# Kernel optimization log

Measured on AMD Instinct MI355X. Metric: run time of the kernel, lower is better.

The kernel has to match this reference:

```python
import jax, jax.numpy as jnp
import numpy as np

D_MODEL = 1024
N_HEADS = 16
D_K = D_MODEL // N_HEADS  # 64
SCALE = 1.0 / np.sqrt(D_K).astype(np.float32)


def setup_inputs() -> dict:
    key = jax.random.key(0)
    kx, kq, kk, kv, ko = jax.random.split(key, 5)
    B, S = 2, 2048
    s = 0.02  # keep pre-softmax logits in a sane range
    return {
        "x": jax.random.normal(kx, (B, S, D_MODEL), dtype=jnp.float32),
        "Wq": jax.random.normal(kq, (D_MODEL, D_MODEL), dtype=jnp.float32) * s,
        "Wk": jax.random.normal(kk, (D_MODEL, D_MODEL), dtype=jnp.float32) * s,
        "Wv": jax.random.normal(kv, (D_MODEL, D_MODEL), dtype=jnp.float32) * s,
        "Wo": jax.random.normal(ko, (D_MODEL, D_MODEL), dtype=jnp.float32) * s,
    }


def reference(x, Wq, Wk, Wv, Wo):
    # x: [B, S, D]; nn.Linear(bias=False) computes x @ W.T
    B, S, D = x.shape
    H, dk = N_HEADS, D_K

    def proj(W):
        # [B, S, D] -> [B, H, S, dk]
        return (x @ W.T).reshape(B, S, H, dk).transpose(0, 2, 1, 3)

    q = proj(Wq)
    k = proj(Wk)
    v = proj(Wv)

    # Flash tiling with online softmax is exact full attention (no mask):
    scores = jnp.einsum("bhqd,bhkd->bhqk", q, k) * SCALE  # [B,H,S,S]
    p = jax.nn.softmax(scores, axis=-1)
    o = jnp.einsum("bhqk,bhkd->bhqd", p, v)               # [B,H,S,dk]

    o = o.transpose(0, 2, 1, 3).reshape(B, S, D)
    return o @ Wo.T
```

## Files before the change

### kernel.cpp

```cpp
#include <hip/hip_runtime.h>
#include <cstdint>
#include <type_traits>

typedef __attribute__((ext_vector_type(8))) __bf16 bf16x8;
typedef __attribute__((ext_vector_type(4))) float f32x4;
using u16 = unsigned short;
using u32 = unsigned int;

#define D_MODEL 1024
#define N_HEADS 16
#define D_K     64
#define SEQ     2048
#define BATCH   2
#define NTOKENS (BATCH * SEQ)
#define SCALE   0.125f
#define LOG2E   1.44269504088896340736f
#define C2      (SCALE * LOG2E)

__device__ __forceinline__ u16 f32_to_bf16(float f) {
    union { float f; u32 u; } v; v.f = f;
    u32 r = (v.u + 0x7fffu + ((v.u >> 16) & 1u)) >> 16;
    return (u16)r;
}

__device__ __forceinline__ u32 pack_bf16_pair(float a, float b) {
    u32 ua = __builtin_bit_cast(u32, a) + 0x8000u;
    u32 ub = __builtin_bit_cast(u32, b) + 0x8000u;
    return __builtin_amdgcn_perm(ub, ua, 0x07060302);
}

typedef const __attribute__((address_space(1))) u32* gas_ptr;
typedef __attribute__((address_space(3))) u32* las_ptr;
__device__ __forceinline__ void gl2lds16(const u16* g, u16* l) {
    __builtin_amdgcn_global_load_lds((gas_ptr)g, (las_ptr)l, 16, 0, 0);
}

__global__ __launch_bounds__(256) void cvt_all(const float* __restrict__ x,
                                               const float* __restrict__ Wq, const float* __restrict__ Wk,
                                               const float* __restrict__ Wv, const float* __restrict__ Wo,
                                               u16* __restrict__ xb,
                                               u16* __restrict__ wq, u16* __restrict__ wk,
                                               u16* __restrict__ wv, u16* __restrict__ wo) {
    const int NX = NTOKENS * D_MODEL;
    size_t i = (size_t)(blockIdx.x * 256 + threadIdx.x) * 4;
    const float* src; u16* dst; size_t off;
    if (i < (size_t)NX) { src = x; dst = xb; off = i; }
    else {
        size_t j = i - NX;
        int w = (int)(j >> 20);
        off = j & ((1u << 20) - 1);
        src = (w == 0) ? Wq : (w == 1) ? Wk : (w == 2) ? Wv : Wo;
        dst = (w == 0) ? wq : (w == 1) ? wk : (w == 2) ? wv : wo;
    }
    float4 f = *(const float4*)(src + off);
    u32 lo = (u32)f32_to_bf16(f.x) | ((u32)f32_to_bf16(f.y) << 16);
    u32 hi = (u32)f32_to_bf16(f.z) | ((u32)f32_to_bf16(f.w) << 16);
    uint2 o; o.x = lo; o.y = hi;
    *(uint2*)(dst + off) = o;
}

__global__ __launch_bounds__(256) void gemm_qkv(const u16* __restrict__ xb,
                                                const u16* __restrict__ wq,
                                                const u16* __restrict__ wk,
                                                const u16* __restrict__ wv,
                                                u16* __restrict__ Qb, u16* __restrict__ Kb,
                                                u16* __restrict__ Vt) {
    __shared__ __align__(16) u16 As[2][128 * 32];
    __shared__ __align__(16) u16 Bs[2][128 * 32];

    const int tid  = threadIdx.x;
    const int wave = tid >> 6, lane = tid & 63;
    const int quad = lane >> 4, l4 = lane & 15;
    const int wm = wave >> 1, wn = wave & 1;
    const int f = blockIdx.x;

    const u16 *Abase, *Bbase;
    if (f < 512) {
        const int m0 = (f & 31) * 128, t = f >> 5;
        Abase = xb + (size_t)m0 * D_MODEL;
        Bbase = ((t < 8) ? wq : wk) + (size_t)(t & 7) * 128 * D_MODEL;
    } else {
        const int g = f - 512;
        Abase = wv + (size_t)(g & 7) * 128 * D_MODEL;
        Bbase = xb + (size_t)(g >> 3) * 128 * D_MODEL;
    }

    f32x4 acc[4][4] = {};

    const int r0 = wave * 16 + (lane >> 2);
    const int ch = (lane & 3) * 8;
    const u16* Ag0 = Abase + (size_t)r0 * D_MODEL + ch;
    const u16* Bg0 = Bbase + (size_t)r0 * D_MODEL + ch;
    u16* AsW0 = As[0] + wave * 512;
    u16* AsW1 = As[1] + wave * 512;
    u16* BsW0 = Bs[0] + wave * 512;
    u16* BsW1 = Bs[1] + wave * 512;

    for (int kt = 0; kt < 16; ++kt) {
        const int ko = kt * 64;
        __syncthreads();
        gl2lds16(Ag0 + ko, AsW0);
        gl2lds16(Ag0 + (size_t)64 * D_MODEL + ko, AsW0 + 2048);
        gl2lds16(Bg0 + ko, BsW0);
        gl2lds16(Bg0 + (size_t)64 * D_MODEL + ko, BsW0 + 2048);
        gl2lds16(Ag0 + ko + 32, AsW1);
        gl2lds16(Ag0 + (size_t)64 * D_MODEL + ko + 32, AsW1 + 2048);
        gl2lds16(Bg0 + ko + 32, BsW1);
        gl2lds16(Bg0 + (size_t)64 * D_MODEL + ko + 32, BsW1 + 2048);
        __syncthreads();

#pragma unroll
        for (int s = 0; s < 2; ++s) {
            bf16x8 af[4], bfr[4];
#pragma unroll
            for (int mt = 0; mt < 4; mt++)
                af[mt] = *(const bf16x8*)&As[s][(wm * 64 + mt * 16 + l4) * 32 + quad * 8];
#pragma unroll
            for (int nt = 0; nt < 4; nt++)
                bfr[nt] = *(const bf16x8*)&Bs[s][(wn * 64 + nt * 16 + l4) * 32 + quad * 8];
#pragma unroll
            for (int mt = 0; mt < 4; mt++)
#pragma unroll
                for (int nt = 0; nt < 4; nt++)
                    acc[mt][nt] = __builtin_amdgcn_mfma_f32_16x16x32_bf16(af[mt], bfr[nt], acc[mt][nt], 0, 0, 0);
        }
    }

#pragma unroll
    for (int mt = 0; mt < 4; mt++)
#pragma unroll
        for (int nt = 0; nt < 4; nt++)
#pragma unroll
            for (int r = 0; r < 4; r++) {
                int mrow = wm * 64 + mt * 16 + quad * 4 + r;
                int ncol = wn * 64 + nt * 16 + l4;
                float v = acc[mt][nt][r];
                if (f < 512) {
                    const int m0 = (f & 31) * 128, t = f >> 5;
                    if (t < 8)
                        Qb[(size_t)(m0 + mrow) * D_MODEL + (t & 7) * 128 + ncol] = f32_to_bf16(v * C2);
                    else
                        Kb[(size_t)(m0 + mrow) * D_MODEL + (t & 7) * 128 + ncol] = f32_to_bf16(v);
                } else {
                    const int g = f - 512;
                    Vt[(size_t)((g & 7) * 128 + mrow) * NTOKENS + (g >> 3) * 128 + ncol] = f32_to_bf16(v);
                }
            }
}

__global__ __launch_bounds__(256) void gemm_out(const u16* __restrict__ A,
                                                const u16* __restrict__ Bw,
                                                float* __restrict__ C) {
    __shared__ __align__(16) u16 As[64 * 32];
    __shared__ __align__(16) u16 Bs[128 * 32];

    const int tid  = threadIdx.x;
    const int wave = tid >> 6, lane = tid & 63;
    const int quad = lane >> 4, l4 = lane & 15;
    const int m0 = blockIdx.y * 64, n0 = blockIdx.x * 128;

    f32x4 acc[4][2] = {};

    const int r0 = wave * 16 + (lane >> 2);
    const int ch = (lane & 3) * 8;
    const u16* Ag0 = A  + (size_t)(m0 + r0) * D_MODEL + ch;
    const u16* Bg0 = Bw + (size_t)(n0 + r0) * D_MODEL + ch;
    u16* AsW = As + wave * 512;
    u16* BsW = Bs + wave * 512;

    for (int kt = 0; kt < 32; ++kt) {
        const int ko = kt * 32;
        __syncthreads();
        gl2lds16(Ag0 + ko, AsW);
        gl2lds16(Bg0 + ko, BsW);
        gl2lds16(Bg0 + (size_t)64 * D_MODEL + ko, BsW + 2048);
        __syncthreads();

        bf16x8 af[4], bfr[2];
#pragma unroll
        for (int mt = 0; mt < 4; mt++)
            af[mt] = *(const bf16x8*)&As[(mt * 16 + l4) * 32 + quad * 8];
#pragma unroll
        for (int nt = 0; nt < 2; nt++)
            bfr[nt] = *(const bf16x8*)&Bs[(wave * 32 + nt * 16 + l4) * 32 + quad * 8];
#pragma unroll
        for (int mt = 0; mt < 4; mt++)
#pragma unroll
            for (int nt = 0; nt < 2; nt++)
                acc[mt][nt] = __builtin_amdgcn_mfma_f32_16x16x32_bf16(af[mt], bfr[nt], acc[mt][nt], 0, 0, 0);
    }

#pragma unroll
    for (int mt = 0; mt < 4; mt++)
#pragma unroll
        for (int nt = 0; nt < 2; nt++)
#pragma unroll
            for (int r = 0; r < 4; r++) {
                int m = m0 + mt * 16 + quad * 4 + r;
                int n = n0 + wave * 32 + nt * 16 + l4;
                C[(size_t)m * D_MODEL + n] = acc[mt][nt][r];
            }
}

__global__ __launch_bounds__(512, 4) void attn(const u16* __restrict__ Q,
                                               const u16* __restrict__ K,
                                               const u16* __restrict__ Vt,
                                               u16* __restrict__ O) {
    __shared__ __align__(16) u16 smem[2 * 64 * 72 + 2 * 80 * 72];
    u16* KsB = smem;
    u16* VsB = smem + 2 * 64 * 72;
    const int KBUF = 64 * 72, VBUF = 80 * 72;

    const int tid  = threadIdx.x;
    const int wave = tid >> 6, lane = tid & 63;
    const int quad = lane >> 4, l4 = lane & 15;
    const int qg = wave & 3, kv = wave >> 2;
    const int bid = blockIdx.x;
    const int h  = (bid & 7) | (((bid >> 3) & 1) << 3);
    const int b  = (bid >> 4) & 1;
    const int q0 = (bid >> 5) * 128;
    const size_t headoff = (size_t)b * SEQ * D_MODEL + (size_t)h * D_K;

    for (int i = tid; i < 2 * 16 * 72; i += 512) {
        int buf = i / (16 * 72), rem = i % (16 * 72);
        VsB[buf * VBUF + (64 + rem / 72) * 72 + (rem % 72)] = (rem / 72 == 0) ? (u16)0x3F80 : (u16)0;
    }

    const int sarr = tid >> 8;
    const int st   = tid & 255;
    const int srow = st >> 2, sc = st & 3;
    const u16* gsrc = (sarr == 0)
        ? K  + headoff + (size_t)srow * D_MODEL + sc * 16
        : Vt + (size_t)(h * 64 + srow) * NTOKENS + (size_t)b * SEQ + sc * 16;
    const size_t gstep = (sarr == 0) ? (size_t)64 * D_MODEL : 64;
    u16* kw0 = KsB + srow * 72 + sc * 16;
    u16* vw0 = VsB + srow * 72 + (sc >> 1) * 32 + (sc & 1) * 4;

    bf16x8 qa[2][2];
#pragma unroll
    for (int qs = 0; qs < 2; qs++) {
        const u16* qp = Q + headoff + (size_t)(q0 + qg * 32 + qs * 16 + l4) * D_MODEL + quad * 8;
        qa[qs][0] = *(const bf16x8*)qp;
        qa[qs][1] = *(const bf16x8*)(qp + 32);
    }

    int4 pr0 = *(const int4*)gsrc;
    int4 pr1 = *(const int4*)(gsrc + 8);

    f32x4 acc_o[2][4] = {};
    f32x4 acc_l[2] = {};

    for (int it = 0; it < 32; ++it) {
        if (sarr == 0) {
            u16* d = kw0 + (it & 1) * KBUF;
            *(int4*)d       = pr0;
            *(int4*)(d + 8) = pr1;
        } else {
            u16* d = vw0 + (it & 1) * VBUF;
            const uint2* h0 = (const uint2*)&pr0;
            const uint2* h1 = (const uint2*)&pr1;
            *(uint2*)(d)      = h0[0];
            *(uint2*)(d + 8)  = h0[1];
            *(uint2*)(d + 16) = h1[0];
            *(uint2*)(d + 24) = h1[1];
        }
        __syncthreads();

        const u16* gn = gsrc + (size_t)((it + 1) & 31) * gstep;
        pr0 = *(const int4*)gn;
        pr1 = *(const int4*)(gn + 8);

        const u16* ksr = KsB + (it & 1) * KBUF;
        const u16* vsr = VsB + (it & 1) * VBUF;

        f32x4 sacc[2][2] = {};
#pragma unroll
        for (int n2 = 0; n2 < 2; n2++) {
            const int krow = kv * 32 + n2 * 16 + l4;
            bf16x8 kb0 = *(const bf16x8*)&ksr[krow * 72 + quad * 8];
            bf16x8 kb1 = *(const bf16x8*)&ksr[krow * 72 + 32 + quad * 8];
#pragma unroll
            for (int qs = 0; qs < 2; qs++) {
                sacc[qs][n2] = __builtin_amdgcn_mfma_f32_16x16x32_bf16(kb0, qa[qs][0], sacc[qs][n2], 0, 0, 0);
                sacc[qs][n2] = __builtin_amdgcn_mfma_f32_16x16x32_bf16(kb1, qa[qs][1], sacc[qs][n2], 0, 0, 0);
            }
        }

        union { u32 u[4]; bf16x8 v; } pp[2];
#pragma unroll
        for (int qs = 0; qs < 2; qs++)
#pragma unroll
            for (int n2 = 0; n2 < 2; n2++) {
                float p0 = __builtin_amdgcn_exp2f(sacc[qs][n2][0]);
                float p1 = __builtin_amdgcn_exp2f(sacc[qs][n2][1]);
                float p2 = __builtin_amdgcn_exp2f(sacc[qs][n2][2]);
                float p3 = __builtin_amdgcn_exp2f(sacc[qs][n2][3]);
                pp[qs].u[n2 * 2]     = pack_bf16_pair(p0, p1);
                pp[qs].u[n2 * 2 + 1] = pack_bf16_pair(p2, p3);
            }

#pragma unroll
        for (int dvt = 0; dvt < 4; dvt++) {
            bf16x8 vfr = *(const bf16x8*)&vsr[(dvt * 16 + l4) * 72 + kv * 32 + quad * 8];
#pragma unroll
            for (int qs = 0; qs < 2; qs++)
                acc_o[qs][dvt] = __builtin_amdgcn_mfma_f32_16x16x32_bf16(pp[qs].v, vfr, acc_o[qs][dvt], 0, 0, 0);
        }
        {
            bf16x8 ofr = *(const bf16x8*)&vsr[(64 + l4) * 72 + kv * 32 + quad * 8];
#pragma unroll
            for (int qs = 0; qs < 2; qs++)
                acc_l[qs] = __builtin_amdgcn_mfma_f32_16x16x32_bf16(pp[qs].v, ofr, acc_l[qs], 0, 0, 0);
        }
    }

    float* Of = (float*)smem;
    float* Lf = (float*)(smem + 16384);
    __syncthreads();
    if (kv == 1) {
#pragma unroll
        for (int qs = 0; qs < 2; qs++) {
#pragma unroll
            for (int dvt = 0; dvt < 4; dvt++)
#pragma unroll
                for (int r = 0; r < 4; r++)
                    Of[(qg * 32 + qs * 16 + quad * 4 + r) * 64 + dvt * 16 + l4] = acc_o[qs][dvt][r];
            if (l4 == 0)
#pragma unroll
                for (int r = 0; r < 4; r++)
                    Lf[qg * 32 + qs * 16 + quad * 4 + r] = acc_l[qs][r];
        }
    }
    __syncthreads();
    if (kv == 0) {
#pragma unroll
        for (int qs = 0; qs < 2; qs++)
#pragma unroll
            for (int r = 0; r < 4; r++) {
                float lown = __shfl(acc_l[qs][r], quad * 16, 64);
                float ltot = lown + Lf[qg * 32 + qs * 16 + quad * 4 + r];
                float linv = 1.f / ltot;
                int qrow = q0 + qg * 32 + qs * 16 + quad * 4 + r;
#pragma unroll
                for (int dvt = 0; dvt < 4; dvt++) {
                    float v = acc_o[qs][dvt][r] +
                              Of[(qg * 32 + qs * 16 + quad * 4 + r) * 64 + dvt * 16 + l4];
                    O[headoff + (size_t)qrow * D_MODEL + dvt * 16 + l4] = f32_to_bf16(v * linv);
                }
            }
    }
}

extern "C" void kernel_launch(void* const* d_in, const int* in_sizes, int n_in,
                              void* d_out, int out_size, void* d_ws, size_t ws_size,
                              hipStream_t stream) {
    const float* x  = (const float*)d_in[0];
    const float* Wq = (const float*)d_in[1];
    const float* Wk = (const float*)d_in[2];
    const float* Wv = (const float*)d_in[3];
    const float* Wo = (const float*)d_in[4];

    const int NW = D_MODEL * D_MODEL;

    char* ws = (char*)d_ws;
    u16* xb = (u16*)ws;
    u16* wq = (u16*)(ws + (8u << 20));
    u16* wk = wq + NW;
    u16* wv = wk + NW;
    u16* wo = wv + NW;
    u16* Qb  = (u16*)(ws + (16u << 20));
    u16* Kb  = (u16*)(ws + (24u << 20));
    u16* Vtb = (u16*)(ws + (32u << 20));

    cvt_all<<<8192, 256, 0, stream>>>(x, Wq, Wk, Wv, Wo, xb, wq, wk, wv, wo);

    gemm_qkv<<<768, 256, 0, stream>>>(xb, wq, wk, wv, Qb, Kb, Vtb);

    attn<<<512, 512, 0, stream>>>(Qb, Kb, Vtb, xb);

    gemm_out<<<dim3(8, 64), 256, 0, stream>>>(xb, wo, (float*)d_out);
}
```

Baseline: 188.8 us.

## Retile attention and output GEMM, use hardware bf16 pack and MFMA priority

The attention kernel moves from 512-thread blocks (4 query groups × 2 KV halves) to 256-thread blocks in which each wave handles all 64 queries of a block against its own quarter of a 128-key tile. The row-sum now uses a register ones vector instead of extra LDS rows, and the partial sums of the four waves are reduced in two stages. The output GEMM grows to 128x128 tiles with a 64-wide K step staged in two LDS halves, and the attention kernel uses v_cvt_pk_bf16_f32 plus s_setprio around its MFMA blocks. The aim is more operand reuse per LDS read and fewer loop iterations and barriers, at the cost of higher register pressure and lower occupancy.

```diff
diff --git a/kernel.cpp b/kernel.cpp
--- a/kernel.cpp
+++ b/kernel.cpp
@@ -1,6 +1,5 @@
 #include <hip/hip_runtime.h>
 #include <cstdint>
-#include <type_traits>
 
 typedef __attribute__((ext_vector_type(8))) __bf16 bf16x8;
 typedef __attribute__((ext_vector_type(4))) float f32x4;
@@ -23,10 +22,10 @@
     return (u16)r;
 }
 
-__device__ __forceinline__ u32 pack_bf16_pair(float a, float b) {
-    u32 ua = __builtin_bit_cast(u32, a) + 0x8000u;
-    u32 ub = __builtin_bit_cast(u32, b) + 0x8000u;
-    return __builtin_amdgcn_perm(ub, ua, 0x07060302);
+__device__ __forceinline__ u32 cvt_pk_bf16(float a, float b) {
+    u32 r;
+    asm("v_cvt_pk_bf16_f32 %0, %1, %2" : "=v"(r) : "v"(a), "v"(b));
+    return r;
 }
 
 typedef const __attribute__((address_space(1))) u32* gas_ptr;
@@ -151,200 +150,264 @@
 __global__ __launch_bounds__(256) void gemm_out(const u16* __restrict__ A,
                                                 const u16* __restrict__ Bw,
                                                 float* __restrict__ C) {
-    __shared__ __align__(16) u16 As[64 * 32];
-    __shared__ __align__(16) u16 Bs[128 * 32];
+    __shared__ __align__(16) u16 As[2][128 * 32];
+    __shared__ __align__(16) u16 Bs[2][128 * 32];
 
     const int tid  = threadIdx.x;
     const int wave = tid >> 6, lane = tid & 63;
     const int quad = lane >> 4, l4 = lane & 15;
-    const int m0 = blockIdx.y * 64, n0 = blockIdx.x * 128;
-
-    f32x4 acc[4][2] = {};
+    const int wm = wave >> 1, wn = wave & 1;
+    const int m0 = (blockIdx.x & 31) * 128, n0 = (blockIdx.x >> 5) * 128;
+
+    f32x4 acc[4][4] = {};
 
     const int r0 = wave * 16 + (lane >> 2);
     const int ch = (lane & 3) * 8;
     const u16* Ag0 = A  + (size_t)(m0 + r0) * D_MODEL + ch;
     const u16* Bg0 = Bw + (size_t)(n0 + r0) * D_MODEL + ch;
-    u16* AsW = As + wave * 512;
-    u16* BsW = Bs + wave * 512;
-
-    for (int kt = 0; kt < 32; ++kt) {
-        const int ko = kt * 32;
+    u16* AsW0 = As[0] + wave * 512;
+    u16* AsW1 = As[1] + wave * 512;
+    u16* BsW0 = Bs[0] + wave * 512;
+    u16* BsW1 = Bs[1] + wave * 512;
+
+    for (int kt = 0; kt < 16; ++kt) {
+        const int ko = kt * 64;
         __syncthreads();
-        gl2lds16(Ag0 + ko, AsW);
-        gl2lds16(Bg0 + ko, BsW);
-        gl2lds16(Bg0 + (size_t)64 * D_MODEL + ko, BsW + 2048);
+        gl2lds16(Ag0 + ko, AsW0);
+        gl2lds16(Ag0 + (size_t)64 * D_MODEL + ko, AsW0 + 2048);
+        gl2lds16(Bg0 + ko, BsW0);
+        gl2lds16(Bg0 + (size_t)64 * D_MODEL + ko, BsW0 + 2048);
+        gl2lds16(Ag0 + ko + 32, AsW1);
+        gl2lds16(Ag0 + (size_t)64 * D_MODEL + ko + 32, AsW1 + 2048);
+        gl2lds16(Bg0 + ko + 32, BsW1);
+        gl2lds16(Bg0 + (size_t)64 * D_MODEL + ko + 32, BsW1 + 2048);
         __syncthreads();
 
-        bf16x8 af[4], bfr[2];
-#pragma unroll
-        for (int mt = 0; mt < 4; mt++)
-            af[mt] = *(const bf16x8*)&As[(mt * 16 + l4) * 32 + quad * 8];
-#pragma unroll
-        for (int nt = 0; nt < 2; nt++)
-            bfr[nt] = *(const bf16x8*)&Bs[(wave * 32 + nt * 16 + l4) * 32 + quad * 8];
-#pragma unroll
-        for (int mt = 0; mt < 4; mt++)
-#pragma unroll
-            for (int nt = 0; nt < 2; nt++)
-                acc[mt][nt] = __builtin_amdgcn_mfma_f32_16x16x32_bf16(af[mt], bfr[nt], acc[mt][nt], 0, 0, 0);
+#pragma unroll
+        for (int s = 0; s < 2; ++s) {
+            bf16x8 af[4], bfr[4];
+#pragma unroll
+            for (int mt = 0; mt < 4; mt++)
+                af[mt] = *(const bf16x8*)&As[s][(wm * 64 + mt * 16 + l4) * 32 + quad * 8];
+#pragma unroll
+            for (int nt = 0; nt < 4; nt++)
+                bfr[nt] = *(const bf16x8*)&Bs[s][(wn * 64 + nt * 16 + l4) * 32 + quad * 8];
+#pragma unroll
+            for (int mt = 0; mt < 4; mt++)
+#pragma unroll
+                for (int nt = 0; nt < 4; nt++)
+                    acc[mt][nt] = __builtin_amdgcn_mfma_f32_16x16x32_bf16(af[mt], bfr[nt], acc[mt][nt], 0, 0, 0);
+        }
     }
 
 #pragma unroll
     for (int mt = 0; mt < 4; mt++)
 #pragma unroll
-        for (int nt = 0; nt < 2; nt++)
+        for (int nt = 0; nt < 4; nt++)
 #pragma unroll
             for (int r = 0; r < 4; r++) {
-                int m = m0 + mt * 16 + quad * 4 + r;
-                int n = n0 + wave * 32 + nt * 16 + l4;
-                C[(size_t)m * D_MODEL + n] = acc[mt][nt][r];
+                int mrow = wm * 64 + mt * 16 + quad * 4 + r;
+                int ncol = wn * 64 + nt * 16 + l4;
+                C[(size_t)(m0 + mrow) * D_MODEL + n0 + ncol] = acc[mt][nt][r];
             }
 }
 
-__global__ __launch_bounds__(512, 4) void attn(const u16* __restrict__ Q,
+__global__ __launch_bounds__(256, 2) void attn(const u16* __restrict__ Q,
                                                const u16* __restrict__ K,
                                                const u16* __restrict__ Vt,
                                                u16* __restrict__ O) {
-    __shared__ __align__(16) u16 smem[2 * 64 * 72 + 2 * 80 * 72];
+    __shared__ __align__(16) u16 smem[2 * 128 * 72 + 2 * 64 * 136];
     u16* KsB = smem;
-    u16* VsB = smem + 2 * 64 * 72;
-    const int KBUF = 64 * 72, VBUF = 80 * 72;
+    u16* VsB = smem + 2 * 128 * 72;
+    const int KBUF = 128 * 72, VBUF = 64 * 136;
 
     const int tid  = threadIdx.x;
-    const int wave = tid >> 6, lane = tid & 63;
+    const int kv   = tid >> 6, lane = tid & 63;
     const int quad = lane >> 4, l4 = lane & 15;
-    const int qg = wave & 3, kv = wave >> 2;
-    const int bid = blockIdx.x;
-    const int h  = (bid & 7) | (((bid >> 3) & 1) << 3);
-    const int b  = (bid >> 4) & 1;
-    const int q0 = (bid >> 5) * 128;
+    const int bid  = blockIdx.x;
+    const int bh   = bid >> 5;
+    const int b    = bh >> 4, h = bh & 15;
+    const int q0   = (bid & 31) * 64;
     const size_t headoff = (size_t)b * SEQ * D_MODEL + (size_t)h * D_K;
 
-    for (int i = tid; i < 2 * 16 * 72; i += 512) {
-        int buf = i / (16 * 72), rem = i % (16 * 72);
-        VsB[buf * VBUF + (64 + rem / 72) * 72 + (rem % 72)] = (rem / 72 == 0) ? (u16)0x3F80 : (u16)0;
-    }
-
-    const int sarr = tid >> 8;
-    const int st   = tid & 255;
-    const int srow = st >> 2, sc = st & 3;
-    const u16* gsrc = (sarr == 0)
-        ? K  + headoff + (size_t)srow * D_MODEL + sc * 16
-        : Vt + (size_t)(h * 64 + srow) * NTOKENS + (size_t)b * SEQ + sc * 16;
-    const size_t gstep = (sarr == 0) ? (size_t)64 * D_MODEL : 64;
+    const int srow = tid >> 2, sc = tid & 3;
+    const u16* gK = K  + headoff + (size_t)srow * D_MODEL + sc * 16;
+    const u16* gV = Vt + (size_t)(h * 64 + srow) * NTOKENS + (size_t)b * SEQ + sc * 16;
     u16* kw0 = KsB + srow * 72 + sc * 16;
-    u16* vw0 = VsB + srow * 72 + (sc >> 1) * 32 + (sc & 1) * 4;
-
-    bf16x8 qa[2][2];
-#pragma unroll
-    for (int qs = 0; qs < 2; qs++) {
-        const u16* qp = Q + headoff + (size_t)(q0 + qg * 32 + qs * 16 + l4) * D_MODEL + quad * 8;
+    u16* vw0 = VsB + srow * 136 + (sc >> 1) * 32 + (sc & 1) * 4;
+
+    bf16x8 qa[4][2];
+#pragma unroll
+    for (int qs = 0; qs < 4; qs++) {
+        const u16* qp = Q + headoff + (size_t)(q0 + qs * 16 + l4) * D_MODEL + quad * 8;
         qa[qs][0] = *(const bf16x8*)qp;
         qa[qs][1] = *(const bf16x8*)(qp + 32);
     }
 
-    int4 pr0 = *(const int4*)gsrc;
-    int4 pr1 = *(const int4*)(gsrc + 8);
-
-    f32x4 acc_o[2][4] = {};
-    f32x4 acc_l[2] = {};
-
-    for (int it = 0; it < 32; ++it) {
-        if (sarr == 0) {
-            u16* d = kw0 + (it & 1) * KBUF;
-            *(int4*)d       = pr0;
-            *(int4*)(d + 8) = pr1;
-        } else {
-            u16* d = vw0 + (it & 1) * VBUF;
-            const uint2* h0 = (const uint2*)&pr0;
-            const uint2* h1 = (const uint2*)&pr1;
-            *(uint2*)(d)      = h0[0];
-            *(uint2*)(d + 8)  = h0[1];
-            *(uint2*)(d + 16) = h1[0];
-            *(uint2*)(d + 24) = h1[1];
+    union { u32 u[4]; bf16x8 v; } onesu;
+#pragma unroll
+    for (int i = 0; i < 4; i++) onesu.u[i] = 0x3F803F80u;
+
+    int4 pk[4], pv[4];
+    pk[0] = *(const int4*)gK;
+    pk[1] = *(const int4*)(gK + 8);
+    pk[2] = *(const int4*)(gK + (size_t)64 * D_MODEL);
+    pk[3] = *(const int4*)(gK + (size_t)64 * D_MODEL + 8);
+    pv[0] = *(const int4*)gV;
+    pv[1] = *(const int4*)(gV + 8);
+    pv[2] = *(const int4*)(gV + 64);
+    pv[3] = *(const int4*)(gV + 72);
+
+    f32x4 acc_o[4][4] = {};
+    f32x4 acc_l[4] = {};
+
+    for (int it = 0; it < 16; ++it) {
+        u16* kd = kw0 + (it & 1) * KBUF;
+        *(int4*)kd = pk[0];
+        *(int4*)(kd + 8) = pk[1];
+        *(int4*)(kd + 64 * 72) = pk[2];
+        *(int4*)(kd + 64 * 72 + 8) = pk[3];
+        u16* vd = vw0 + (it & 1) * VBUF;
+        {
+            const uint2* a0 = (const uint2*)&pv[0];
+            const uint2* a1 = (const uint2*)&pv[1];
+            *(uint2*)(vd)      = a0[0];
+            *(uint2*)(vd + 8)  = a0[1];
+            *(uint2*)(vd + 16) = a1[0];
+            *(uint2*)(vd + 24) = a1[1];
+            const uint2* b0 = (const uint2*)&pv[2];
+            const uint2* b1 = (const uint2*)&pv[3];
+            u16* vd2 = vd + 64;
+            *(uint2*)(vd2)      = b0[0];
+            *(uint2*)(vd2 + 8)  = b0[1];
+            *(uint2*)(vd2 + 16) = b1[0];
+            *(uint2*)(vd2 + 24) = b1[1];
         }
         __syncthreads();
 
-        const u16* gn = gsrc + (size_t)((it + 1) & 31) * gstep;
-        pr0 = *(const int4*)gn;
-        pr1 = *(const int4*)(gn + 8);
+        const int nx = (it + 1) & 15;
+        const u16* gkn = gK + (size_t)nx * 128 * D_MODEL;
+        const u16* gvn = gV + (size_t)nx * 128;
+        pk[0] = *(const int4*)gkn;
+        pk[1] = *(const int4*)(gkn + 8);
+        pk[2] = *(const int4*)(gkn + (size_t)64 * D_MODEL);
+        pk[3] = *(const int4*)(gkn + (size_t)64 * D_MODEL + 8);
+        pv[0] = *(const int4*)gvn;
+        pv[1] = *(const int4*)(gvn + 8);
+        pv[2] = *(const int4*)(gvn + 64);
+        pv[3] = *(const int4*)(gvn + 72);
 
         const u16* ksr = KsB + (it & 1) * KBUF;
         const u16* vsr = VsB + (it & 1) * VBUF;
 
-        f32x4 sacc[2][2] = {};
+        bf16x8 kb[2][2];
 #pragma unroll
         for (int n2 = 0; n2 < 2; n2++) {
             const int krow = kv * 32 + n2 * 16 + l4;
-            bf16x8 kb0 = *(const bf16x8*)&ksr[krow * 72 + quad * 8];
-            bf16x8 kb1 = *(const bf16x8*)&ksr[krow * 72 + 32 + quad * 8];
-#pragma unroll
-            for (int qs = 0; qs < 2; qs++) {
-                sacc[qs][n2] = __builtin_amdgcn_mfma_f32_16x16x32_bf16(kb0, qa[qs][0], sacc[qs][n2], 0, 0, 0);
-                sacc[qs][n2] = __builtin_amdgcn_mfma_f32_16x16x32_bf16(kb1, qa[qs][1], sacc[qs][n2], 0, 0, 0);
+            kb[n2][0] = *(const bf16x8*)&ksr[krow * 72 + quad * 8];
+            kb[n2][1] = *(const bf16x8*)&ksr[krow * 72 + 32 + quad * 8];
+        }
+        f32x4 sacc[4][2] = {};
+        __builtin_amdgcn_s_setprio(1);
+#pragma unroll
+        for (int qs = 0; qs < 4; qs++)
+#pragma unroll
+            for (int n2 = 0; n2 < 2; n2++) {
+                sacc[qs][n2] = __builtin_amdgcn_mfma_f32_16x16x32_bf16(kb[n2][0], qa[qs][0], sacc[qs][n2], 0, 0, 0);
+                sacc[qs][n2] = __builtin_amdgcn_mfma_f32_16x16x32_bf16(kb[n2][1], qa[qs][1], sacc[qs][n2], 0, 0, 0);
             }
-        }
-
-        union { u32 u[4]; bf16x8 v; } pp[2];
-#pragma unroll
-        for (int qs = 0; qs < 2; qs++)
+        __builtin_amdgcn_s_setprio(0);
+
+        union { u32 u[4]; bf16x8 v; } pp[4];
+#pragma unroll
+        for (int qs = 0; qs < 4; qs++)
 #pragma unroll
             for (int n2 = 0; n2 < 2; n2++) {
                 float p0 = __builtin_amdgcn_exp2f(sacc[qs][n2][0]);
                 float p1 = __builtin_amdgcn_exp2f(sacc[qs][n2][1]);
                 float p2 = __builtin_amdgcn_exp2f(sacc[qs][n2][2]);
                 float p3 = __builtin_amdgcn_exp2f(sacc[qs][n2][3]);
-                pp[qs].u[n2 * 2]     = pack_bf16_pair(p0, p1);
-                pp[qs].u[n2 * 2 + 1] = pack_bf16_pair(p2, p3);
+                pp[qs].u[n2 * 2]     = cvt_pk_bf16(p0, p1);
+                pp[qs].u[n2 * 2 + 1] = cvt_pk_bf16(p2, p3);
             }
 
+        __builtin_amdgcn_s_setprio(1);
 #pragma unroll
         for (int dvt = 0; dvt < 4; dvt++) {
-            bf16x8 vfr = *(const bf16x8*)&vsr[(dvt * 16 + l4) * 72 + kv * 32 + quad * 8];
-#pragma unroll
-            for (int qs = 0; qs < 2; qs++)
+            bf16x8 vfr = *(const bf16x8*)&vsr[(dvt * 16 + l4) * 136 + kv * 32 + quad * 8];
+#pragma unroll
+            for (int qs = 0; qs < 4; qs++)
                 acc_o[qs][dvt] = __builtin_amdgcn_mfma_f32_16x16x32_bf16(pp[qs].v, vfr, acc_o[qs][dvt], 0, 0, 0);
         }
-        {
-            bf16x8 ofr = *(const bf16x8*)&vsr[(64 + l4) * 72 + kv * 32 + quad * 8];
-#pragma unroll
-            for (int qs = 0; qs < 2; qs++)
-                acc_l[qs] = __builtin_amdgcn_mfma_f32_16x16x32_bf16(pp[qs].v, ofr, acc_l[qs], 0, 0, 0);
-        }
-    }
-
-    float* Of = (float*)smem;
-    float* Lf = (float*)(smem + 16384);
+#pragma unroll
+        for (int qs = 0; qs < 4; qs++)
+            acc_l[qs] = __builtin_amdgcn_mfma_f32_16x16x32_bf16(pp[qs].v, onesu.v, acc_l[qs], 0, 0, 0);
+        __builtin_amdgcn_s_setprio(0);
+    }
+
+    const int OFS = 68;
+    float* OfA = (float*)smem;
+    float* OfB = OfA + 64 * OFS;
+    float* LA  = OfB + 64 * OFS;
+    float* LB  = LA + 64;
+
     __syncthreads();
-    if (kv == 1) {
-#pragma unroll
-        for (int qs = 0; qs < 2; qs++) {
+    if (kv == 1 || kv == 3) {
+        float* Of = (kv == 1) ? OfA : OfB;
+        float* L  = (kv == 1) ? LA  : LB;
+#pragma unroll
+        for (int qs = 0; qs < 4; qs++) {
 #pragma unroll
             for (int dvt = 0; dvt < 4; dvt++)
 #pragma unroll
                 for (int r = 0; r < 4; r++)
-                    Of[(qg * 32 + qs * 16 + quad * 4 + r) * 64 + dvt * 16 + l4] = acc_o[qs][dvt][r];
+                    Of[(qs * 16 + quad * 4 + r) * OFS + dvt * 16 + l4] = acc_o[qs][dvt][r];
             if (l4 == 0)
 #pragma unroll
                 for (int r = 0; r < 4; r++)
-                    Lf[qg * 32 + qs * 16 + quad * 4 + r] = acc_l[qs][r];
+                    L[qs * 16 + quad * 4 + r] = acc_l[qs][r];
+        }
+    }
+    __syncthreads();
+    if (kv == 2) {
+#pragma unroll
+        for (int qs = 0; qs < 4; qs++) {
+#pragma unroll
+            for (int dvt = 0; dvt < 4; dvt++)
+#pragma unroll
+                for (int r = 0; r < 4; r++)
+                    OfB[(qs * 16 + quad * 4 + r) * OFS + dvt * 16 + l4] += acc_o[qs][dvt][r];
+            if (l4 == 0)
+#pragma unroll
+                for (int r = 0; r < 4; r++)
+                    LB[qs * 16 + quad * 4 + r] += acc_l[qs][r];
+        }
+    } else if (kv == 0) {
+#pragma unroll
+        for (int qs = 0; qs < 4; qs++) {
+#pragma unroll
+            for (int dvt = 0; dvt < 4; dvt++)
+#pragma unroll
+                for (int r = 0; r < 4; r++)
+                    acc_o[qs][dvt][r] += OfA[(qs * 16 + quad * 4 + r) * OFS + dvt * 16 + l4];
+#pragma unroll
+            for (int r = 0; r < 4; r++)
+                acc_l[qs][r] += LA[qs * 16 + quad * 4 + r];
         }
     }
     __syncthreads();
     if (kv == 0) {
 #pragma unroll
-        for (int qs = 0; qs < 2; qs++)
+        for (int qs = 0; qs < 4; qs++)
 #pragma unroll
             for (int r = 0; r < 4; r++) {
-                float lown = __shfl(acc_l[qs][r], quad * 16, 64);
-                float ltot = lown + Lf[qg * 32 + qs * 16 + quad * 4 + r];
+                const int qi = qs * 16 + quad * 4 + r;
+                float ltot = acc_l[qs][r] + LB[qi];
                 float linv = 1.f / ltot;
-                int qrow = q0 + qg * 32 + qs * 16 + quad * 4 + r;
+                const int qrow = q0 + qi;
 #pragma unroll
                 for (int dvt = 0; dvt < 4; dvt++) {
-                    float v = acc_o[qs][dvt][r] +
-                              Of[(qg * 32 + qs * 16 + quad * 4 + r) * 64 + dvt * 16 + l4];
+                    float v = acc_o[qs][dvt][r] + OfB[qi * OFS + dvt * 16 + l4];
                     O[headoff + (size_t)qrow * D_MODEL + dvt * 16 + l4] = f32_to_bf16(v * linv);
                 }
             }
@@ -376,7 +439,7 @@
 
     gemm_qkv<<<768, 256, 0, stream>>>(xb, wq, wk, wv, Qb, Kb, Vtb);
 
-    attn<<<512, 512, 0, stream>>>(Qb, Kb, Vtb, xb);
-
-    gemm_out<<<dim3(8, 64), 256, 0, stream>>>(xb, wo, (float*)d_out);
-}
+    attn<<<1024, 256, 0, stream>>>(Qb, Kb, Vtb, xb);
+
+    gemm_out<<<256, 256, 0, stream>>>(xb, wo, (float*)d_out);
+}
```

New measurement: 239.5 us. 26.9% more time.

## Retile output GEMM, swizzle attention LDS, use hardware bf16 pack and priorities

Applied to the files above, without the earlier changes.

The output projection GEMM moves from 64x128 to 128x128 block tiles with a K step of 64, giving each wave a 64x64 sub-tile and halving the grid. The attention kernel replaces padded 72-stride LDS rows with XOR-swizzled 64-stride rows to avoid bank conflicts. The row-sum MFMA now reads a constant ones register instead of an LDS ones row, and the softmax packing uses the v_cvt_pk_bf16_f32 instruction. s_setprio is wrapped around the MFMA sections. The larger GEMM tiles lower parallelism to 256 blocks, and the packing instruction may round differently from the previous add-and-truncate.

```diff
diff --git a/kernel.cpp b/kernel.cpp
--- a/kernel.cpp
+++ b/kernel.cpp
@@ -1,6 +1,5 @@
 #include <hip/hip_runtime.h>
 #include <cstdint>
-#include <type_traits>
 
 typedef __attribute__((ext_vector_type(8))) __bf16 bf16x8;
 typedef __attribute__((ext_vector_type(4))) float f32x4;
@@ -23,10 +22,10 @@
     return (u16)r;
 }
 
-__device__ __forceinline__ u32 pack_bf16_pair(float a, float b) {
-    u32 ua = __builtin_bit_cast(u32, a) + 0x8000u;
-    u32 ub = __builtin_bit_cast(u32, b) + 0x8000u;
-    return __builtin_amdgcn_perm(ub, ua, 0x07060302);
+__device__ __forceinline__ u32 cvt_pk_bf16(float a, float b) {
+    u32 r;
+    asm("v_cvt_pk_bf16_f32 %0, %1, %2" : "=v"(r) : "v"(a), "v"(b));
+    return r;
 }
 
 typedef const __attribute__((address_space(1))) u32* gas_ptr;
@@ -151,54 +150,65 @@
 __global__ __launch_bounds__(256) void gemm_out(const u16* __restrict__ A,
                                                 const u16* __restrict__ Bw,
                                                 float* __restrict__ C) {
-    __shared__ __align__(16) u16 As[64 * 32];
-    __shared__ __align__(16) u16 Bs[128 * 32];
+    __shared__ __align__(16) u16 As[2][128 * 32];
+    __shared__ __align__(16) u16 Bs[2][128 * 32];
 
     const int tid  = threadIdx.x;
     const int wave = tid >> 6, lane = tid & 63;
     const int quad = lane >> 4, l4 = lane & 15;
-    const int m0 = blockIdx.y * 64, n0 = blockIdx.x * 128;
-
-    f32x4 acc[4][2] = {};
+    const int wm = wave >> 1, wn = wave & 1;
+    const int m0 = (blockIdx.x & 31) * 128, n0 = (blockIdx.x >> 5) * 128;
+
+    f32x4 acc[4][4] = {};
 
     const int r0 = wave * 16 + (lane >> 2);
     const int ch = (lane & 3) * 8;
     const u16* Ag0 = A  + (size_t)(m0 + r0) * D_MODEL + ch;
     const u16* Bg0 = Bw + (size_t)(n0 + r0) * D_MODEL + ch;
-    u16* AsW = As + wave * 512;
-    u16* BsW = Bs + wave * 512;
-
-    for (int kt = 0; kt < 32; ++kt) {
-        const int ko = kt * 32;
+    u16* AsW0 = As[0] + wave * 512;
+    u16* AsW1 = As[1] + wave * 512;
+    u16* BsW0 = Bs[0] + wave * 512;
+    u16* BsW1 = Bs[1] + wave * 512;
+
+    for (int kt = 0; kt < 16; ++kt) {
+        const int ko = kt * 64;
         __syncthreads();
-        gl2lds16(Ag0 + ko, AsW);
-        gl2lds16(Bg0 + ko, BsW);
-        gl2lds16(Bg0 + (size_t)64 * D_MODEL + ko, BsW + 2048);
+        gl2lds16(Ag0 + ko, AsW0);
+        gl2lds16(Ag0 + (size_t)64 * D_MODEL + ko, AsW0 + 2048);
+        gl2lds16(Bg0 + ko, BsW0);
+        gl2lds16(Bg0 + (size_t)64 * D_MODEL + ko, BsW0 + 2048);
+        gl2lds16(Ag0 + ko + 32, AsW1);
+        gl2lds16(Ag0 + (size_t)64 * D_MODEL + ko + 32, AsW1 + 2048);
+        gl2lds16(Bg0 + ko + 32, BsW1);
+        gl2lds16(Bg0 + (size_t)64 * D_MODEL + ko + 32, BsW1 + 2048);
         __syncthreads();
 
-        bf16x8 af[4], bfr[2];
-#pragma unroll
-        for (int mt = 0; mt < 4; mt++)
-            af[mt] = *(const bf16x8*)&As[(mt * 16 + l4) * 32 + quad * 8];
-#pragma unroll
-        for (int nt = 0; nt < 2; nt++)
-            bfr[nt] = *(const bf16x8*)&Bs[(wave * 32 + nt * 16 + l4) * 32 + quad * 8];
-#pragma unroll
-        for (int mt = 0; mt < 4; mt++)
-#pragma unroll
-            for (int nt = 0; nt < 2; nt++)
-                acc[mt][nt] = __builtin_amdgcn_mfma_f32_16x16x32_bf16(af[mt], bfr[nt], acc[mt][nt], 0, 0, 0);
+#pragma unroll
+        for (int s = 0; s < 2; ++s) {
+            bf16x8 af[4], bfr[4];
+#pragma unroll
+            for (int mt = 0; mt < 4; mt++)
+                af[mt] = *(const bf16x8*)&As[s][(wm * 64 + mt * 16 + l4) * 32 + quad * 8];
+#pragma unroll
+            for (int nt = 0; nt < 4; nt++)
+                bfr[nt] = *(const bf16x8*)&Bs[s][(wn * 64 + nt * 16 + l4) * 32 + quad * 8];
+#pragma unroll
+            for (int mt = 0; mt < 4; mt++)
+#pragma unroll
+                for (int nt = 0; nt < 4; nt++)
+                    acc[mt][nt] = __builtin_amdgcn_mfma_f32_16x16x32_bf16(af[mt], bfr[nt], acc[mt][nt], 0, 0, 0);
+        }
     }
 
 #pragma unroll
     for (int mt = 0; mt < 4; mt++)
 #pragma unroll
-        for (int nt = 0; nt < 2; nt++)
+        for (int nt = 0; nt < 4; nt++)
 #pragma unroll
             for (int r = 0; r < 4; r++) {
-                int m = m0 + mt * 16 + quad * 4 + r;
-                int n = n0 + wave * 32 + nt * 16 + l4;
-                C[(size_t)m * D_MODEL + n] = acc[mt][nt][r];
+                int mrow = wm * 64 + mt * 16 + quad * 4 + r;
+                int ncol = wn * 64 + nt * 16 + l4;
+                C[(size_t)(m0 + mrow) * D_MODEL + n0 + ncol] = acc[mt][nt][r];
             }
 }
 
@@ -206,10 +216,10 @@
                                                const u16* __restrict__ K,
                                                const u16* __restrict__ Vt,
                                                u16* __restrict__ O) {
-    __shared__ __align__(16) u16 smem[2 * 64 * 72 + 2 * 80 * 72];
+    __shared__ __align__(16) u16 smem[17664];
     u16* KsB = smem;
-    u16* VsB = smem + 2 * 64 * 72;
-    const int KBUF = 64 * 72, VBUF = 80 * 72;
+    u16* VsB = smem + 8192;
+    const int KBUF = 4096, VBUF = 4096;
 
     const int tid  = threadIdx.x;
     const int wave = tid >> 6, lane = tid & 63;
@@ -221,20 +231,22 @@
     const int q0 = (bid >> 5) * 128;
     const size_t headoff = (size_t)b * SEQ * D_MODEL + (size_t)h * D_K;
 
-    for (int i = tid; i < 2 * 16 * 72; i += 512) {
-        int buf = i / (16 * 72), rem = i % (16 * 72);
-        VsB[buf * VBUF + (64 + rem / 72) * 72 + (rem % 72)] = (rem / 72 == 0) ? (u16)0x3F80 : (u16)0;
-    }
-
     const int sarr = tid >> 8;
     const int st   = tid & 255;
     const int srow = st >> 2, sc = st & 3;
+    const int r7   = srow & 7;
     const u16* gsrc = (sarr == 0)
         ? K  + headoff + (size_t)srow * D_MODEL + sc * 16
         : Vt + (size_t)(h * 64 + srow) * NTOKENS + (size_t)b * SEQ + sc * 16;
     const size_t gstep = (sarr == 0) ? (size_t)64 * D_MODEL : 64;
-    u16* kw0 = KsB + srow * 72 + sc * 16;
-    u16* vw0 = VsB + srow * 72 + (sc >> 1) * 32 + (sc & 1) * 4;
+
+    const int kd0 = srow * 64 + (((2 * sc)     ^ r7) * 8);
+    const int kd1 = srow * 64 + (((2 * sc + 1) ^ r7) * 8);
+    const int g32 = sc >> 1, vc = sc & 1;
+    const int vw0 = srow * 64 + (((g32 * 4 + 0) ^ r7) * 8) + 4 * vc;
+    const int vw1 = srow * 64 + (((g32 * 4 + 1) ^ r7) * 8) + 4 * vc;
+    const int vw2 = srow * 64 + (((g32 * 4 + 2) ^ r7) * 8) + 4 * vc;
+    const int vw3 = srow * 64 + (((g32 * 4 + 3) ^ r7) * 8) + 4 * vc;
 
     bf16x8 qa[2][2];
 #pragma unroll
@@ -244,25 +256,31 @@
         qa[qs][1] = *(const bf16x8*)(qp + 32);
     }
 
+    union { u32 u[4]; bf16x8 v; } onesu;
+#pragma unroll
+    for (int i = 0; i < 4; i++) onesu.u[i] = 0x3F803F80u;
+
     int4 pr0 = *(const int4*)gsrc;
     int4 pr1 = *(const int4*)(gsrc + 8);
 
     f32x4 acc_o[2][4] = {};
     f32x4 acc_l[2] = {};
 
+    const int sw7 = l4 & 7;
+
     for (int it = 0; it < 32; ++it) {
         if (sarr == 0) {
-            u16* d = kw0 + (it & 1) * KBUF;
-            *(int4*)d       = pr0;
-            *(int4*)(d + 8) = pr1;
+            u16* d = KsB + (it & 1) * KBUF;
+            *(int4*)(d + kd0) = pr0;
+            *(int4*)(d + kd1) = pr1;
         } else {
-            u16* d = vw0 + (it & 1) * VBUF;
+            u16* d = VsB + (it & 1) * VBUF;
             const uint2* h0 = (const uint2*)&pr0;
             const uint2* h1 = (const uint2*)&pr1;
-            *(uint2*)(d)      = h0[0];
-            *(uint2*)(d + 8)  = h0[1];
-            *(uint2*)(d + 16) = h1[0];
-            *(uint2*)(d + 24) = h1[1];
+            *(uint2*)(d + vw0) = h0[0];
+            *(uint2*)(d + vw1) = h0[1];
+            *(uint2*)(d + vw2) = h1[0];
+            *(uint2*)(d + vw3) = h1[1];
         }
         __syncthreads();
 
@@ -273,18 +291,23 @@
         const u16* ksr = KsB + (it & 1) * KBUF;
         const u16* vsr = VsB + (it & 1) * VBUF;
 
-        f32x4 sacc[2][2] = {};
+        bf16x8 kb[2][2];
 #pragma unroll
         for (int n2 = 0; n2 < 2; n2++) {
             const int krow = kv * 32 + n2 * 16 + l4;
-            bf16x8 kb0 = *(const bf16x8*)&ksr[krow * 72 + quad * 8];
-            bf16x8 kb1 = *(const bf16x8*)&ksr[krow * 72 + 32 + quad * 8];
-#pragma unroll
-            for (int qs = 0; qs < 2; qs++) {
-                sacc[qs][n2] = __builtin_amdgcn_mfma_f32_16x16x32_bf16(kb0, qa[qs][0], sacc[qs][n2], 0, 0, 0);
-                sacc[qs][n2] = __builtin_amdgcn_mfma_f32_16x16x32_bf16(kb1, qa[qs][1], sacc[qs][n2], 0, 0, 0);
+            kb[n2][0] = *(const bf16x8*)&ksr[krow * 64 + ((quad       ^ sw7) * 8)];
+            kb[n2][1] = *(const bf16x8*)&ksr[krow * 64 + (((4 + quad) ^ sw7) * 8)];
+        }
+        f32x4 sacc[2][2] = {};
+        __builtin_amdgcn_s_setprio(1);
+#pragma unroll
+        for (int qs = 0; qs < 2; qs++)
+#pragma unroll
+            for (int n2 = 0; n2 < 2; n2++) {
+                sacc[qs][n2] = __builtin_amdgcn_mfma_f32_16x16x32_bf16(kb[n2][0], qa[qs][0], sacc[qs][n2], 0, 0, 0);
+                sacc[qs][n2] = __builtin_amdgcn_mfma_f32_16x16x32_bf16(kb[n2][1], qa[qs][1], sacc[qs][n2], 0, 0, 0);
             }
-        }
+        __builtin_amdgcn_s_setprio(0);
 
         union { u32 u[4]; bf16x8 v; } pp[2];
 #pragma unroll
@@ -295,27 +318,28 @@
                 float p1 = __builtin_amdgcn_exp2f(sacc[qs][n2][1]);
                 float p2 = __builtin_amdgcn_exp2f(sacc[qs][n2][2]);
                 float p3 = __builtin_amdgcn_exp2f(sacc[qs][n2][3]);
-                pp[qs].u[n2 * 2]     = pack_bf16_pair(p0, p1);
-                pp[qs].u[n2 * 2 + 1] = pack_bf16_pair(p2, p3);
+                pp[qs].u[n2 * 2]     = cvt_pk_bf16(p0, p1);
+                pp[qs].u[n2 * 2 + 1] = cvt_pk_bf16(p2, p3);
             }
 
+        __builtin_amdgcn_s_setprio(1);
 #pragma unroll
         for (int dvt = 0; dvt < 4; dvt++) {
-            bf16x8 vfr = *(const bf16x8*)&vsr[(dvt * 16 + l4) * 72 + kv * 32 + quad * 8];
+            const int vrow = dvt * 16 + l4;
+            bf16x8 vfr = *(const bf16x8*)&vsr[vrow * 64 + ((((kv << 2) + quad) ^ sw7) * 8)];
 #pragma unroll
             for (int qs = 0; qs < 2; qs++)
                 acc_o[qs][dvt] = __builtin_amdgcn_mfma_f32_16x16x32_bf16(pp[qs].v, vfr, acc_o[qs][dvt], 0, 0, 0);
         }
-        {
-            bf16x8 ofr = *(const bf16x8*)&vsr[(64 + l4) * 72 + kv * 32 + quad * 8];
-#pragma unroll
-            for (int qs = 0; qs < 2; qs++)
-                acc_l[qs] = __builtin_amdgcn_mfma_f32_16x16x32_bf16(pp[qs].v, ofr, acc_l[qs], 0, 0, 0);
-        }
-    }
-
+#pragma unroll
+        for (int qs = 0; qs < 2; qs++)
+            acc_l[qs] = __builtin_amdgcn_mfma_f32_16x16x32_bf16(pp[qs].v, onesu.v, acc_l[qs], 0, 0, 0);
+        __builtin_amdgcn_s_setprio(0);
+    }
+
+    const int OFS = 68;
     float* Of = (float*)smem;
-    float* Lf = (float*)(smem + 16384);
+    float* Lf = Of + 128 * OFS;
     __syncthreads();
     if (kv == 1) {
 #pragma unroll
@@ -324,7 +348,7 @@
             for (int dvt = 0; dvt < 4; dvt++)
 #pragma unroll
                 for (int r = 0; r < 4; r++)
-                    Of[(qg * 32 + qs * 16 + quad * 4 + r) * 64 + dvt * 16 + l4] = acc_o[qs][dvt][r];
+                    Of[(qg * 32 + qs * 16 + quad * 4 + r) * OFS + dvt * 16 + l4] = acc_o[qs][dvt][r];
             if (l4 == 0)
 #pragma unroll
                 for (int r = 0; r < 4; r++)
@@ -337,14 +361,13 @@
         for (int qs = 0; qs < 2; qs++)
 #pragma unroll
             for (int r = 0; r < 4; r++) {
-                float lown = __shfl(acc_l[qs][r], quad * 16, 64);
-                float ltot = lown + Lf[qg * 32 + qs * 16 + quad * 4 + r];
+                const int qi = qg * 32 + qs * 16 + quad * 4 + r;
+                float ltot = acc_l[qs][r] + Lf[qi];
                 float linv = 1.f / ltot;
-                int qrow = q0 + qg * 32 + qs * 16 + quad * 4 + r;
+                const int qrow = q0 + qi;
 #pragma unroll
                 for (int dvt = 0; dvt < 4; dvt++) {
-                    float v = acc_o[qs][dvt][r] +
-                              Of[(qg * 32 + qs * 16 + quad * 4 + r) * 64 + dvt * 16 + l4];
+                    float v = acc_o[qs][dvt][r] + Of[qi * OFS + dvt * 16 + l4];
                     O[headoff + (size_t)qrow * D_MODEL + dvt * 16 + l4] = f32_to_bf16(v * linv);
                 }
             }
@@ -378,5 +401,5 @@
 
     attn<<<512, 512, 0, stream>>>(Qb, Kb, Vtb, xb);
 
-    gemm_out<<<dim3(8, 64), 256, 0, stream>>>(xb, wo, (float*)d_out);
-}
+    gemm_out<<<256, 256, 0, stream>>>(xb, wo, (float*)d_out);
+}
```

Result: faster. 183.4 us (-2.9%).
